# Optimization experiments

Hardware: AMD Instinct MI355X
Metric: run time of the kernel (lower is better)

## Reference

```python
import math
import jax, jax.numpy as jnp
import numpy as np

D_MODEL = 1024
D_STATE = 16
D_CONV = 4
EXPAND = 2
N_MOD = 2
D_INNER = EXPAND * D_MODEL
DT_RANK = math.ceil(D_MODEL / 16)
B_SZ = 2
SEQLEN = 2048


def setup_inputs() -> dict:
    key = jax.random.key(0)
    ks = jax.random.split(key, 10)
    hidden_states = jax.random.normal(ks[0], (B_SZ, SEQLEN, D_MODEL), jnp.float32)
    modality_ids = jax.random.randint(ks[1], (B_SZ, SEQLEN), 0, N_MOD).astype(jnp.int32)
    W_in = jax.random.normal(ks[2], (N_MOD, 2 * D_INNER, D_MODEL), jnp.float32) * (D_MODEL ** -0.5)
    conv_w = jax.random.normal(ks[3], (D_INNER, D_CONV), jnp.float32) * (D_CONV ** -0.5)
    conv_b = jnp.zeros((D_INNER,), jnp.float32)
    W_x = jax.random.normal(ks[4], (N_MOD, DT_RANK + 2 * D_STATE, D_INNER), jnp.float32) * (D_INNER ** -0.5)
    dt_init_std = DT_RANK ** -0.5
    W_dt = jax.random.uniform(ks[5], (N_MOD, D_INNER, DT_RANK), jnp.float32, -dt_init_std, dt_init_std)
    # dt bias init: inverse-softplus of dt ~ LogUniform(dt_min, dt_max), per Mamba
    dt = jnp.exp(jax.random.uniform(ks[6], (N_MOD, D_INNER), jnp.float32)
                 * (math.log(0.1) - math.log(0.001)) + math.log(0.001))
    dt = jnp.maximum(dt, 1e-4)
    b_dt = dt + jnp.log(-jnp.expm1(-dt))
    A_log = jnp.log(jnp.broadcast_to(jnp.arange(1, D_STATE + 1, dtype=jnp.float32), (D_INNER, D_STATE)))
    D = jnp.ones((D_INNER,), jnp.float32)
    W_out = jax.random.normal(ks[7], (N_MOD, D_MODEL, D_INNER), jnp.float32) * (D_INNER ** -0.5)
    return dict(hidden_states=hidden_states, modality_ids=modality_ids, W_in=W_in,
                conv_w=conv_w, conv_b=conv_b, W_x=W_x, W_dt=W_dt, b_dt=b_dt,
                A_log=A_log, D=D, W_out=W_out)


def _expert_apply(x, W, ids):
    # x: [T, d_in], W: [E, d_out, d_in], ids: [T] -> per-token expert output [T, d_out]
    all_out = jnp.einsum('td,eod->teo', x, W)
    return jnp.take_along_axis(all_out, ids[:, None, None], axis=1)[:, 0, :]


def _forward(hidden_states, modality_ids, W_in, conv_w, conv_b, W_x, W_dt, b_dt, A_log, D, W_out):
    Bsz, L, d_model = hidden_states.shape
    d_inner, d_state = A_log.shape
    dt_rank = W_dt.shape[2]
    d_conv = conv_w.shape[1]
    ids = modality_ids.reshape(-1)  # [T]

    # per-modality in_proj dispatch/combine
    xz = _expert_apply(hidden_states.reshape(-1, d_model), W_in, ids)  # [T, 2*d_inner]
    xz = xz.reshape(Bsz, L, 2 * d_inner).transpose(0, 2, 1)            # [B, 2*d_inner, L]
    x, z = jnp.split(xz, 2, axis=1)                                    # [B, d_inner, L] each

    # causal depthwise conv1d (pad left d_conv-1, truncate to L) + SiLU
    xp = jnp.pad(x, ((0, 0), (0, 0), (d_conv - 1, 0)))
    xc = conv_b[None, :, None]
    for k in range(d_conv):
        xc = xc + conv_w[None, :, k:k + 1] * xp[:, :, k:k + L]
    x = jax.nn.silu(xc)

    # per-modality x_proj -> (dt, B, C)
    xt = x.transpose(0, 2, 1).reshape(-1, d_inner)                     # [T, d_inner]
    x_dbl = _expert_apply(xt, W_x, ids)
    dt, Bm, Cm = jnp.split(x_dbl, [dt_rank, dt_rank + d_state], axis=-1)

    # per-modality dt_proj (with bias), then softplus (delta_softplus=True)
    dt = _expert_apply(dt, W_dt, ids) + b_dt[ids]                      # [T, d_inner]
    dt = jax.nn.softplus(dt)

    A = -jnp.exp(A_log)                                                # [d_inner, d_state]

    # selective scan over sequence (time-major)
    dts = dt.reshape(Bsz, L, d_inner).transpose(1, 0, 2)               # [L, B, d_inner]
    Bms = Bm.reshape(Bsz, L, d_state).transpose(1, 0, 2)               # [L, B, d_state]
    Cms = Cm.reshape(Bsz, L, d_state).transpose(1, 0, 2)               # [L, B, d_state]
    xs = x.transpose(2, 0, 1)                                          # [L, B, d_inner]

    def step(state, inp):
        x_t, dt_t, B_t, C_t = inp
        dA = jnp.exp(dt_t[..., None] * A)                              # [B, d_inner, d_state]
        state = state * dA + (dt_t * x_t)[..., None] * B_t[:, None, :]
        y_t = jnp.einsum('bdn,bn->bd', state, C_t)
        return state, y_t

    init = jnp.zeros((Bsz, d_inner, d_state), jnp.float32)
    _, ys = jax.lax.scan(step, init, (xs, dts, Bms, Cms))              # ys: [L, B, d_inner]

    y = ys.transpose(1, 0, 2)                                          # [B, L, d_inner]
    y = y + x.transpose(0, 2, 1) * D[None, None, :]                    # skip D*u
    y = y * jax.nn.silu(z.transpose(0, 2, 1))                          # z gate

    # per-modality out_proj
    out = _expert_apply(y.reshape(-1, d_inner), W_out, ids)
    return out.reshape(Bsz, L, d_model)


def reference(hidden_states, modality_ids, W_in, conv_w, conv_b, W_x, W_dt, b_dt, A_log, D, W_out):
    return _forward(hidden_states, modality_ids, W_in, conv_w, conv_b, W_x, W_dt, b_dt, A_log, D, W_out)
```

## Files before the change

### kernel.cpp

```cpp
#include <hip/hip_runtime.h>
#include <hip/hip_bf16.h>
#include <math.h>

#define B_SZ 2
#define SEQLEN 2048
#define D_MODEL 1024
#define D_INNER 2048
#define D_STATE 16
#define D_CONV 4
#define DT_RANK 64
#define NTOK (B_SZ * SEQLEN)
#define XDBL 96
#define NC 32
#define LC 64
#define PADTOT (17 * 256)

typedef float f32x4 __attribute__((ext_vector_type(4)));
typedef unsigned int u32x4 __attribute__((ext_vector_type(4)));
typedef __hip_bfloat16 bf16;

__device__ __forceinline__ float siluf(float v) { return v / (1.f + __expf(-v)); }
__device__ __forceinline__ float softplusf(float v) { return (v > 20.f) ? v : log1pf(__expf(v)); }

__device__ __forceinline__ void mfma_bf16(f32x4& acc, u32x4 a, u32x4 b) {
  asm volatile("v_mfma_f32_16x16x32_bf16 %0, %1, %2, %0" : "+v"(acc) : "v"(a), "v"(b));
}

__device__ __forceinline__ void gload16(const bf16* g, bf16* l) {
  __builtin_amdgcn_global_load_lds(
      (const __attribute__((address_space(1))) unsigned int*)g,
      (__attribute__((address_space(3))) unsigned int*)l, 16, 0, 0);
}

__global__ __launch_bounds__(1024) void k_perm(const int* __restrict__ ids, int* __restrict__ perm) {
  __shared__ int sc[1024];
  const int tid = threadIdx.x;
  int loc[4];
  int cnt = 0;
#pragma unroll
  for (int q = 0; q < 4; q++) {
    loc[q] = ids[tid * 4 + q];
    cnt += (loc[q] == 0);
  }
  sc[tid] = cnt;
  __syncthreads();
  for (int off = 1; off < 1024; off <<= 1) {
    int v = sc[tid];
    int u = (tid >= off) ? sc[tid - off] : 0;
    __syncthreads();
    sc[tid] = v + u;
    __syncthreads();
  }
  const int N0 = sc[1023];
  const int m0 = (N0 + 255) & ~255;
  const int N1 = NTOK - N0;
  for (int idx = tid; idx < PADTOT; idx += 1024)
    if ((idx >= N0 && idx < m0) || idx >= m0 + N1) perm[idx] = -1;
  int zb = sc[tid] - cnt;
#pragma unroll
  for (int q = 0; q < 4; q++) {
    int t = tid * 4 + q;
    if (loc[q] == 0) { perm[zb] = t; zb++; }
    else             { perm[m0 + (t - zb)] = t; }
  }
}

#define CVT_H   (NTOK * D_MODEL)
#define CVT_WIN (2 * 2 * D_INNER * D_MODEL)
#define CVT_WX  (2 * XDBL * D_INNER)
#define CVT_WDT (2 * D_INNER * DT_RANK)
#define CVT_WO  (2 * D_MODEL * D_INNER)
#define CVT_TOT (CVT_H + CVT_WIN + CVT_WX + CVT_WDT + CVT_WO)
__global__ __launch_bounds__(256) void k_cvtall(const float* __restrict__ h,
                                                const float* __restrict__ Win,
                                                const float* __restrict__ Wx,
                                                const float* __restrict__ Wdt,
                                                const float* __restrict__ Wout,
                                                bf16* __restrict__ hB, bf16* __restrict__ WinB,
                                                bf16* __restrict__ WxB, bf16* __restrict__ WdtB,
                                                bf16* __restrict__ WoB) {
  size_t i = ((size_t)blockIdx.x * 256 + threadIdx.x) * 8;
  const float* src; bf16* dst; size_t off;
  if (i < CVT_H)                          { src = h;    dst = hB;   off = i; }
  else if (i < CVT_H + CVT_WIN)           { src = Win;  dst = WinB; off = i - CVT_H; }
  else if (i < CVT_H + CVT_WIN + CVT_WX)  { src = Wx;   dst = WxB;  off = i - CVT_H - CVT_WIN; }
  else if (i < CVT_TOT - CVT_WO)          { src = Wdt;  dst = WdtB; off = i - CVT_H - CVT_WIN - CVT_WX; }
  else                                    { src = Wout; dst = WoB;  off = i - (CVT_TOT - CVT_WO); }
  float4 f0 = *(const float4*)&src[off];
  float4 f1 = *(const float4*)&src[off + 4];
  __align__(16) bf16 tmp[8];
  tmp[0] = __float2bfloat16(f0.x); tmp[1] = __float2bfloat16(f0.y);
  tmp[2] = __float2bfloat16(f0.z); tmp[3] = __float2bfloat16(f0.w);
  tmp[4] = __float2bfloat16(f1.x); tmp[5] = __float2bfloat16(f1.y);
  tmp[6] = __float2bfloat16(f1.z); tmp[7] = __float2bfloat16(f1.w);
  *(u32x4*)&dst[off] = *(const u32x4*)tmp;
}

template <int KDIM, int NW, int KSPLIT, int EPI>
__device__ __forceinline__ void gemmP_body(const bf16* __restrict__ actB,
                                           const int* __restrict__ perm,
                                           const int* __restrict__ ids,
                                           const bf16* __restrict__ WB,
                                           bf16* __restrict__ outx,
                                           bf16* __restrict__ outz,
                                           float* __restrict__ out0) {
  constexpr int KLEN = KDIM / KSPLIT;
  constexpr int NT = KLEN / 64;
  constexpr int NCOL = (EPI == 1) ? (D_MODEL / 128) : 0;
  __shared__ bf16 As[3][256 * 64];
  __shared__ bf16 Ws[3][128 * 64];
  const int tid = threadIdx.x;

  const int gx = gridDim.x;
  const int nwg = gx * gridDim.y;
  const int fid = blockIdx.y * gx + blockIdx.x;
  const int q8 = nwg >> 3;
  const int swz = (fid & 7) * q8 + (fid >> 3);
  const int bx = swz % gx, by = swz / gx;
  const int ot = (KSPLIT > 1) ? (bx % NCOL) * 128 : bx * 128;
  const int kz = (KSPLIT > 1) ? bx / NCOL : 0;
  const int kbase = kz * KLEN;
  const int tt = by * 256;

  const int lane = tid & 63, w = tid >> 6;
  const int wr = w >> 1, wc = w & 1;
  const int lr = lane & 15, lg = lane >> 4;

  const int t00 = perm[tt];
  const int eu = (t00 >= 0) ? ids[t00] : 0;
  const size_t wexp = (size_t)eu * NW * KDIM;

  const int kswz = ((lane & 7) ^ ((lane >> 3) & 7)) * 8;
  size_t aBase[4]; int aLds[4];
  size_t bBase[2]; int bLds[2];
#pragma unroll
  for (int v = 0; v < 4; v++) {
    const int row = w * 32 + v * 8 + (lane >> 3);
    int ta = perm[tt + row]; if (ta < 0) ta = 0;
    aBase[v] = (size_t)ta * KDIM + kswz;
    aLds[v] = (w * 32 + v * 8) * 64;
  }
#pragma unroll
  for (int v = 0; v < 2; v++) {
    const int row = w * 16 + v * 8 + (lane >> 3);
    bBase[v] = wexp + (size_t)(ot + row) * KDIM + kswz;
    bLds[v] = (w * 16 + v * 8) * 64;
  }

  f32x4 acc[4][4];
#pragma unroll
  for (int i = 0; i < 4; i++)
#pragma unroll
    for (int j = 0; j < 4; j++) acc[i][j] = (f32x4){0.f, 0.f, 0.f, 0.f};

#pragma unroll
  for (int kt = 0; kt < 2; kt++) {
    const int k0 = kbase + kt * 64;
    gload16(&actB[aBase[0] + k0], &As[kt][aLds[0]]);
    gload16(&actB[aBase[1] + k0], &As[kt][aLds[1]]);
    gload16(&actB[aBase[2] + k0], &As[kt][aLds[2]]);
    gload16(&actB[aBase[3] + k0], &As[kt][aLds[3]]);
    gload16(&WB[bBase[0] + k0], &Ws[kt][bLds[0]]);
    gload16(&WB[bBase[1] + k0], &Ws[kt][bLds[1]]);
  }

  int bR = 0, bS = 2;
  for (int kt = 0; kt < NT; ++kt) {
    const int kp = kbase + (kt + 2) * 64;
    const bool st = (kt + 2 < NT);
    if (st) {
      gload16(&actB[aBase[0] + kp], &As[bS][aLds[0]]);
      gload16(&actB[aBase[1] + kp], &As[bS][aLds[1]]);
      gload16(&WB[bBase[0] + kp], &Ws[bS][bLds[0]]);
    }
    if (kt < NT - 2)       asm volatile("s_waitcnt vmcnt(9)" ::: "memory");
    else if (kt == NT - 2) asm volatile("s_waitcnt vmcnt(6)" ::: "memory");
    else                   asm volatile("s_waitcnt vmcnt(0)" ::: "memory");
    asm volatile("s_barrier" ::: "memory");

    const bf16* Ab = As[bR];
    const bf16* Wb = Ws[bR];
    u32x4 a[4][2], b0[2][2];
#pragma unroll
    for (int f = 0; f < 4; f++)
#pragma unroll
      for (int s = 0; s < 2; s++) {
        const int row = wr * 64 + f * 16 + lr;
        a[f][s] = *(const u32x4*)&Ab[row * 64 + ((s * 4 + lg) ^ (row & 7)) * 8];
      }
#pragma unroll
    for (int j = 0; j < 2; j++)
#pragma unroll
      for (int s = 0; s < 2; s++) {
        const int row = wc * 64 + j * 16 + lr;
        b0[j][s] = *(const u32x4*)&Wb[row * 64 + ((s * 4 + lg) ^ (row & 7)) * 8];
      }
    __builtin_amdgcn_s_setprio(1);
#pragma unroll
    for (int f = 0; f < 4; f++)
#pragma unroll
      for (int j = 0; j < 2; j++) {
        mfma_bf16(acc[f][j], a[f][0], b0[j][0]);
        mfma_bf16(acc[f][j], a[f][1], b0[j][1]);
      }
    __builtin_amdgcn_s_setprio(0);

    if (st) {
      gload16(&actB[aBase[2] + kp], &As[bS][aLds[2]]);
      gload16(&actB[aBase[3] + kp], &As[bS][aLds[3]]);
      gload16(&WB[bBase[1] + kp], &Ws[bS][bLds[1]]);
    }
    u32x4 b1[2][2];
#pragma unroll
    for (int j = 0; j < 2; j++)
#pragma unroll
      for (int s = 0; s < 2; s++) {
        const int row = wc * 64 + (2 + j) * 16 + lr;
        b1[j][s] = *(const u32x4*)&Wb[row * 64 + ((s * 4 + lg) ^ (row & 7)) * 8];
      }
    __builtin_amdgcn_s_setprio(1);
#pragma unroll
    for (int f = 0; f < 4; f++)
#pragma unroll
      for (int j = 0; j < 2; j++) {
        mfma_bf16(acc[f][2 + j], a[f][0], b1[j][0]);
        mfma_bf16(acc[f][2 + j], a[f][1], b1[j][1]);
      }
    __builtin_amdgcn_s_setprio(0);
    asm volatile("s_waitcnt lgkmcnt(0)" ::: "memory");
    asm volatile("s_barrier" ::: "memory");
    bR = (bR == 2) ? 0 : bR + 1;
    bS = (bS == 2) ? 0 : bS + 1;
  }

#pragma unroll
  for (int i = 0; i < 4; i++) {
#pragma unroll
    for (int r = 0; r < 4; r++) {
      const int m = wr * 64 + i * 16 + lg * 4 + r;
      const int t = perm[tt + m];
      if (t < 0) continue;
#pragma unroll
      for (int j = 0; j < 4; j++) {
        const int col = ot + wc * 64 + j * 16 + lr;
        const float v = acc[i][j][r];
        if (EPI == 0) {
          const bf16 vb = __float2bfloat16(v);
          if (col < D_INNER) outx[(size_t)t * D_INNER + col] = vb;
          else outz[(size_t)t * D_INNER + (col - D_INNER)] = vb;
        } else {
          out0[((size_t)kz * NTOK + t) * D_MODEL + col] = v;
        }
      }
    }
  }
}

__global__ __launch_bounds__(512) void k_inproj(const bf16* actB, const int* perm, const int* ids,
                                                const bf16* WB, bf16* outx, bf16* outz) {
  gemmP_body<D_MODEL, 2 * D_INNER, 1, 0>(actB, perm, ids, WB, outx, outz, nullptr);
}
__global__ __launch_bounds__(512) void k_outproj(const bf16* actB, const int* perm, const int* ids,
                                                 const bf16* WB, float* out0) {
  gemmP_body<D_INNER, D_MODEL, 2, 1>(actB, perm, ids, WB, nullptr, nullptr, out0);
}

__global__ __launch_bounds__(256) void k_xdblg(const bf16* __restrict__ actB,
                                               const int* __restrict__ perm,
                                               const int* __restrict__ ids,
                                               const bf16* __restrict__ WB,
                                               float* __restrict__ out0) {
  constexpr int KDIM = D_INNER, NW = XDBL, LDO = XDBL, KSPLIT = 8;
  constexpr int KLEN = KDIM / KSPLIT;
  __shared__ bf16 As[128 * 64];
  __shared__ bf16 Ws[128 * 64];
  __shared__ int permL[128];
  const int tid = threadIdx.x;
  const int bx = blockIdx.x, by = blockIdx.y;

  const int ot = 0;
  const int kz = bx;
  const int kbase = kz * KLEN;
  const int tt = by * 128;

  if (tid < 128) permL[tid] = perm[tt + tid];

  const int lane = tid & 63, w = tid >> 6;
  const int wr = w >> 1, wc = w & 1;
  const int lr = lane & 15, lg = lane >> 4;

  const int t00 = perm[tt];
  const int eu = (t00 >= 0) ? ids[t00] : 0;
  const size_t wexp = (size_t)eu * NW * KDIM;

  const int srow = w * 32 + (lane >> 3);
  const int scol = (lane & 7) * 8;
  size_t abase[4], bbase[4];
  int ldsoff[4];
#pragma unroll
  for (int v = 0; v < 4; v++) {
    const int row = srow + v * 8;
    int ta = perm[tt + row];
    if (ta < 0) ta = 0;
    abase[v] = (size_t)ta * KDIM + scol;
    int orow = ot + row;
    orow = (orow < NW) ? orow : (NW - 1);
    bbase[v] = wexp + (size_t)orow * KDIM + scol;
    ldsoff[v] = (w * 32 + v * 8) * 64;
  }

  f32x4 acc[4][4];
#pragma unroll
  for (int i = 0; i < 4; i++)
#pragma unroll
    for (int j = 0; j < 4; j++) acc[i][j] = (f32x4){0.f, 0.f, 0.f, 0.f};

  for (int k0 = kbase; k0 < kbase + KLEN; k0 += 64) {
#pragma unroll
    for (int v = 0; v < 4; v++) {
      gload16(&actB[abase[v] + k0], &As[ldsoff[v]]);
      gload16(&WB[bbase[v] + k0], &Ws[ldsoff[v]]);
    }
    __syncthreads();
#pragma unroll
    for (int ks = 0; ks < 64; ks += 32) {
      u32x4 a[4], b[4];
#pragma unroll
      for (int f = 0; f < 4; f++)
        a[f] = *(const u32x4*)&As[(wr * 64 + f * 16 + lr) * 64 + ks + lg * 8];
#pragma unroll
      for (int f = 0; f < 4; f++)
        b[f] = *(const u32x4*)&Ws[(wc * 64 + f * 16 + lr) * 64 + ks + lg * 8];
#pragma unroll
      for (int i = 0; i < 4; i++)
#pragma unroll
        for (int j = 0; j < 4; j++) mfma_bf16(acc[i][j], a[i], b[j]);
    }
    __syncthreads();
  }

#pragma unroll
  for (int i = 0; i < 4; i++) {
#pragma unroll
    for (int r = 0; r < 4; r++) {
      const int m = wr * 64 + i * 16 + lg * 4 + r;
      const int t = permL[m];
      if (t < 0) continue;
#pragma unroll
      for (int j = 0; j < 4; j++) {
        const int col = ot + wc * 64 + j * 16 + lr;
        if (col < NW) out0[((size_t)kz * NTOK + t) * LDO + col] = acc[i][j][r];
      }
    }
  }
}

__global__ __launch_bounds__(256) void k_dtv(const float* __restrict__ xdbl,
                                             const int* __restrict__ perm,
                                             const int* __restrict__ ids,
                                             const float* __restrict__ Wdt,
                                             const float* __restrict__ bdt,
                                             bf16* __restrict__ dtB) {
  const int tid = threadIdx.x;
  const int idx = blockIdx.y * 256 + tid;
  int t = perm[idx];
  const bool act = (t >= 0);
  if (!act) t = 0;
  const int t0 = perm[blockIdx.y * 256];
  const int e = (t0 >= 0) ? ids[t0] : 0;
  float xs[64];
#pragma unroll
  for (int k4 = 0; k4 < 16; k4++) {
    float4 v = *(const float4*)&xdbl[(size_t)t * XDBL + k4 * 4];
    xs[k4 * 4 + 0] = v.x; xs[k4 * 4 + 1] = v.y;
    xs[k4 * 4 + 2] = v.z; xs[k4 * 4 + 3] = v.w;
  }
  const int cbase = blockIdx.x * 64;
  const float* Wb = Wdt + ((size_t)e * D_INNER + cbase) * DT_RANK;
  const float* bb = bdt + (size_t)e * D_INNER + cbase;
#pragma unroll 1
  for (int cc = 0; cc < 8; cc++) {
    __align__(16) bf16 outv[8];
#pragma unroll
    for (int c8 = 0; c8 < 8; c8++) {
      const int c = cc * 8 + c8;
      const float* wrow = Wb + (size_t)c * DT_RANK;
      float acc = bb[c];
#pragma unroll
      for (int k = 0; k < 64; k++) acc = fmaf(xs[k], wrow[k], acc);
      outv[c8] = __float2bfloat16(softplusf(acc));
    }
    if (act) *(u32x4*)&dtB[(size_t)t * D_INNER + cbase + cc * 8] = *(const u32x4*)outv;
  }
}

__global__ __launch_bounds__(256) void k_xred(const float* __restrict__ part,
                                              float* __restrict__ xdbl) {
  const int i = blockIdx.x * 256 + threadIdx.x;
  float s = 0.f;
#pragma unroll
  for (int k = 0; k < 8; k++) s += part[(size_t)k * NTOK * XDBL + i];
  xdbl[i] = s;
}

__global__ __launch_bounds__(256) void k_ored2(const float* __restrict__ part,
                                               float* __restrict__ out) {
  const size_t base = ((size_t)blockIdx.x * 256 + threadIdx.x) * 4;
  constexpr size_t NM = (size_t)NTOK * D_MODEL;
  float4 s = *(const float4*)&part[base];
  float4 p = *(const float4*)&part[NM + base];
  s.x += p.x; s.y += p.y; s.z += p.z; s.w += p.w;
  *(float4*)&out[base] = s;
}

__global__ __launch_bounds__(256) void k_conv(const bf16* __restrict__ xrawB,
                                              const float* __restrict__ cw,
                                              const float* __restrict__ cb,
                                              bf16* __restrict__ xB) {
  int idx = blockIdx.x * 256 + threadIdx.x;
  int c = idx & (D_INNER - 1);
  int t = idx >> 11;
  int l = t & (SEQLEN - 1);
  int b = t >> 11;
  float acc = cb[c];
#pragma unroll
  for (int k = 0; k < D_CONV; k++) {
    int ll = l + k - (D_CONV - 1);
    if (ll >= 0)
      acc = fmaf(cw[c * D_CONV + k],
                 __bfloat162float(xrawB[((size_t)(b * SEQLEN + ll)) * D_INNER + c]), acc);
  }
  xB[(size_t)idx] = __float2bfloat16(siluf(acc));
}

__global__ __launch_bounds__(256) void k_scan_part(const bf16* __restrict__ xB,
                                                   const bf16* __restrict__ dtB,
                                                   const float* __restrict__ xdbl,
                                                   const float* __restrict__ A_log,
                                                   float* __restrict__ F,
                                                   float* __restrict__ Sdt) {
  __shared__ float Bs[LC][D_STATE];
  const int tid = threadIdx.x;
  const int j = blockIdx.y;
  const int ch = blockIdx.x * 256 + tid;
  const int b = ch >> 11, c = ch & (D_INNER - 1);
  const int t0 = (b << 11) + j * LC;
  {
    int l = tid >> 2, q = (tid & 3) * 4;
    *(float4*)&Bs[l][q] = *(const float4*)&xdbl[(size_t)(t0 + l) * XDBL + DT_RANK + q];
  }
  float Ar[D_STATE];
#pragma unroll
  for (int n4 = 0; n4 < 4; n4++) {
    float4 a = *(const float4*)&A_log[(size_t)c * D_STATE + n4 * 4];
    Ar[n4 * 4 + 0] = -__expf(a.x); Ar[n4 * 4 + 1] = -__expf(a.y);
    Ar[n4 * 4 + 2] = -__expf(a.z); Ar[n4 * 4 + 3] = -__expf(a.w);
  }
  __syncthreads();
  float st[D_STATE];
#pragma unroll
  for (int n = 0; n < D_STATE; n++) st[n] = 0.f;
  float sdt = 0.f;
  float dtc = __bfloat162float(dtB[(size_t)t0 * D_INNER + c]);
  float xc = __bfloat162float(xB[(size_t)t0 * D_INNER + c]);
  for (int l = 0; l < LC; l++) {
    float dtn = 0.f, xn = 0.f;
    if (l < LC - 1) {
      dtn = __bfloat162float(dtB[(size_t)(t0 + l + 1) * D_INNER + c]);
      xn = __bfloat162float(xB[(size_t)(t0 + l + 1) * D_INNER + c]);
    }
    const float dtx = dtc * xc;
    sdt += dtc;
#pragma unroll
    for (int n = 0; n < D_STATE; n++) {
      float dA = __expf(dtc * Ar[n]);
      st[n] = fmaf(st[n], dA, dtx * Bs[l][n]);
    }
    dtc = dtn; xc = xn;
  }
  const size_t fb = ((size_t)j * NTOK + ch) * D_STATE;
#pragma unroll
  for (int n4 = 0; n4 < 4; n4++)
    *(float4*)&F[fb + n4 * 4] = make_float4(st[n4 * 4], st[n4 * 4 + 1], st[n4 * 4 + 2], st[n4 * 4 + 3]);
  Sdt[(size_t)j * NTOK + ch] = sdt;
}

__global__ __launch_bounds__(256) void k_combine(const float* __restrict__ F,
                                                 const float* __restrict__ Sdt,
                                                 const float* __restrict__ A_log,
                                                 float* __restrict__ s0) {
  const int gid = blockIdx.x * 256 + threadIdx.x;
  const int ch = gid >> 4, n = gid & 15, c = ch & (D_INNER - 1);
  const float Ar = -__expf(A_log[(size_t)c * D_STATE + n]);
  float s = 0.f;
  for (int j = 0; j < NC; j++) {
    s0[((size_t)j * NTOK + ch) * D_STATE + n] = s;
    s = fmaf(s, __expf(Ar * Sdt[(size_t)j * NTOK + ch]), F[((size_t)j * NTOK + ch) * D_STATE + n]);
  }
}

__global__ __launch_bounds__(256) void k_scan_fin(const bf16* __restrict__ xB,
                                                  const bf16* __restrict__ dtB,
                                                  const float* __restrict__ xdbl,
                                                  const bf16* __restrict__ zB,
                                                  const float* __restrict__ A_log,
                                                  const float* __restrict__ Dp,
                                                  const float* __restrict__ s0,
                                                  bf16* __restrict__ ybuf) {
  __shared__ float Bs[LC][D_STATE];
  __shared__ float Cs[LC][D_STATE];
  const int tid = threadIdx.x;
  const int j = blockIdx.y;
  const int ch = blockIdx.x * 256 + tid;
  const int b = ch >> 11, c = ch & (D_INNER - 1);
  const int t0 = (b << 11) + j * LC;
  {
    int l = tid >> 2, q = (tid & 3) * 4;
    *(float4*)&Bs[l][q] = *(const float4*)&xdbl[(size_t)(t0 + l) * XDBL + DT_RANK + q];
    *(float4*)&Cs[l][q] = *(const float4*)&xdbl[(size_t)(t0 + l) * XDBL + DT_RANK + D_STATE + q];
  }
  float Ar[D_STATE];
#pragma unroll
  for (int n4 = 0; n4 < 4; n4++) {
    float4 a = *(const float4*)&A_log[(size_t)c * D_STATE + n4 * 4];
    Ar[n4 * 4 + 0] = -__expf(a.x); Ar[n4 * 4 + 1] = -__expf(a.y);
    Ar[n4 * 4 + 2] = -__expf(a.z); Ar[n4 * 4 + 3] = -__expf(a.w);
  }
  __syncthreads();
  float st[D_STATE];
  const size_t sb = ((size_t)j * NTOK + ch) * D_STATE;
#pragma unroll
  for (int n4 = 0; n4 < 4; n4++) {
    float4 s = *(const float4*)&s0[sb + n4 * 4];
    st[n4 * 4 + 0] = s.x; st[n4 * 4 + 1] = s.y; st[n4 * 4 + 2] = s.z; st[n4 * 4 + 3] = s.w;
  }
  const float Dc = Dp[c];
  float dtc = __bfloat162float(dtB[(size_t)t0 * D_INNER + c]);
  float xc = __bfloat162float(xB[(size_t)t0 * D_INNER + c]);
  for (int l = 0; l < LC; l++) {
    float dtn = 0.f, xn = 0.f;
    if (l < LC - 1) {
      dtn = __bfloat162float(dtB[(size_t)(t0 + l + 1) * D_INNER + c]);
      xn = __bfloat162float(xB[(size_t)(t0 + l + 1) * D_INNER + c]);
    }
    const float zv = __bfloat162float(zB[(size_t)(t0 + l) * D_INNER + c]);
    const float dtx = dtc * xc;
    float y = 0.f;
#pragma unroll
    for (int n = 0; n < D_STATE; n++) {
      float dA = __expf(dtc * Ar[n]);
      st[n] = fmaf(st[n], dA, dtx * Bs[l][n]);
      y = fmaf(st[n], Cs[l][n], y);
    }
    float yv = fmaf(xc, Dc, y);
    ybuf[(size_t)(t0 + l) * D_INNER + c] = __float2bfloat16(yv * siluf(zv));
    dtc = dtn; xc = xn;
  }
}

extern "C" void kernel_launch(void* const* d_in, const int* in_sizes, int n_in,
                              void* d_out, int out_size, void* d_ws, size_t ws_size,
                              hipStream_t stream) {
  const float* h = (const float*)d_in[0];
  const int* ids = (const int*)d_in[1];
  const float* Win = (const float*)d_in[2];
  const float* cw = (const float*)d_in[3];
  const float* cb = (const float*)d_in[4];
  const float* Wx = (const float*)d_in[5];
  const float* Wdt = (const float*)d_in[6];
  const float* bdt = (const float*)d_in[7];
  const float* Alog = (const float*)d_in[8];
  const float* Dp = (const float*)d_in[9];
  const float* Wout = (const float*)d_in[10];
  float* out = (float*)d_out;

  const size_t NTD = (size_t)NTOK * D_INNER;
  float* ws = (float*)d_ws;
  float* slot0 = ws + 0 * NTD;
  float* slot1 = ws + 1 * NTD;
  float* slot2 = ws + 2 * NTD;
  float* slot3 = ws + 3 * NTD;
  size_t cur = 4 * NTD;
  float* xdbl_p = ws + cur; cur += (size_t)NTOK * XDBL;
  float* sdt_p = ws + cur; cur += (size_t)NC * NTOK;
  int* perm = (int*)(ws + cur); cur += PADTOT;
  bf16* xB = (bf16*)(ws + cur); cur += NTD / 2;
  bf16* WoB = (bf16*)(ws + cur); cur += CVT_WO / 2;
  bf16* WxB = (bf16*)(ws + cur); cur += CVT_WX / 2;
  bf16* WdtB = (bf16*)(ws + cur); cur += CVT_WDT / 2;

  bf16* hB = (bf16*)slot0;
  bf16* dtbB = (bf16*)slot0;
  bf16* zB = (bf16*)slot1;
  bf16* WinB = (bf16*)slot2;
  float* part = slot2;
  float* part2 = slot1;
  bf16* xrawB = (bf16*)slot3;
  float* F = slot3;
  bf16* yB = (bf16*)slot3;
  float* s0 = (float*)d_out;

  k_perm<<<1, 1024, 0, stream>>>(ids, perm);
  k_cvtall<<<CVT_TOT / 8 / 256, 256, 0, stream>>>(h, Win, Wx, Wdt, Wout, hB, WinB, WxB, WdtB, WoB);
  k_inproj<<<dim3(32, 17), 512, 0, stream>>>(hB, perm, ids, WinB, xrawB, zB);
  k_conv<<<NTD / 256, 256, 0, stream>>>(xrawB, cw, cb, xB);
  k_xdblg<<<dim3(8, 34), 256, 0, stream>>>(xB, perm, ids, WxB, part);
  k_xred<<<NTOK * XDBL / 256, 256, 0, stream>>>(part, xdbl_p);
  k_dtv<<<dim3(32, 17), 256, 0, stream>>>(xdbl_p, perm, ids, Wdt, bdt, dtbB);
  k_scan_part<<<dim3(16, NC), 256, 0, stream>>>(xB, dtbB, xdbl_p, Alog, F, sdt_p);
  k_combine<<<256, 256, 0, stream>>>(F, sdt_p, Alog, s0);
  k_scan_fin<<<dim3(16, NC), 256, 0, stream>>>(xB, dtbB, xdbl_p, zB, Alog, Dp, s0, yB);
  k_outproj<<<dim3(16, 17), 512, 0, stream>>>(yB, perm, ids, WoB, part2);
  k_ored2<<<NTOK * D_MODEL / 4 / 256, 256, 0, stream>>>(part2, out);
}
```

Before: 365.9 us.

## Tile dt projection through shared memory with 4x4 register blocking

```diff
diff --git a/kernel.cpp b/kernel.cpp
--- a/kernel.cpp
+++ b/kernel.cpp
@@ -361,36 +361,59 @@
                                              const float* __restrict__ Wdt,
                                              const float* __restrict__ bdt,
                                              bf16* __restrict__ dtB) {
+  __shared__ float Xs[64][65];
+  __shared__ float Ws[64][65];
+  __shared__ int permL[64];
   const int tid = threadIdx.x;
-  const int idx = blockIdx.y * 256 + tid;
-  int t = perm[idx];
-  const bool act = (t >= 0);
-  if (!act) t = 0;
-  const int t0 = perm[blockIdx.y * 256];
+  const int tt = blockIdx.y * 64;
+  const int cb = blockIdx.x * 64;
+  if (tid < 64) permL[tid] = perm[tt + tid];
+  const int t0 = perm[tt];
   const int e = (t0 >= 0) ? ids[t0] : 0;
-  float xs[64];
+  {
+    const int r = tid >> 2, q = (tid & 3) * 16;
+    int ta = perm[tt + r];
+    if (ta < 0) ta = 0;
+    const float* xsrc = &xdbl[(size_t)ta * XDBL + q];
+    const float* wsrc = &Wdt[((size_t)e * D_INNER + cb + r) * DT_RANK + q];
+#pragma unroll
+    for (int u = 0; u < 4; u++) {
+      float4 xv = *(const float4*)&xsrc[u * 4];
+      float4 wv = *(const float4*)&wsrc[u * 4];
+      *(float4*)&Xs[r][q + u * 4] = xv;
+      *(float4*)&Ws[r][q + u * 4] = wv;
+    }
+  }
+  __syncthreads();
+  const int tl = (tid & 15) * 4;
+  const int cl = (tid >> 4) * 4;
+  float acc[4][4] = {};
 #pragma unroll
   for (int k4 = 0; k4 < 16; k4++) {
-    float4 v = *(const float4*)&xdbl[(size_t)t * XDBL + k4 * 4];
-    xs[k4 * 4 + 0] = v.x; xs[k4 * 4 + 1] = v.y;
-    xs[k4 * 4 + 2] = v.z; xs[k4 * 4 + 3] = v.w;
-  }
-  const int cbase = blockIdx.x * 64;
-  const float* Wb = Wdt + ((size_t)e * D_INNER + cbase) * DT_RANK;
-  const float* bb = bdt + (size_t)e * D_INNER + cbase;
-#pragma unroll 1
-  for (int cc = 0; cc < 8; cc++) {
-    __align__(16) bf16 outv[8];
-#pragma unroll
-    for (int c8 = 0; c8 < 8; c8++) {
-      const int c = cc * 8 + c8;
-      const float* wrow = Wb + (size_t)c * DT_RANK;
-      float acc = bb[c];
-#pragma unroll
-      for (int k = 0; k < 64; k++) acc = fmaf(xs[k], wrow[k], acc);
-      outv[c8] = __float2bfloat16(softplusf(acc));
-    }
-    if (act) *(u32x4*)&dtB[(size_t)t * D_INNER + cbase + cc * 8] = *(const u32x4*)outv;
+    float4 xv[4], wv[4];
+#pragma unroll
+    for (int i = 0; i < 4; i++) xv[i] = *(const float4*)&Xs[tl + i][k4 * 4];
+#pragma unroll
+    for (int j = 0; j < 4; j++) wv[j] = *(const float4*)&Ws[cl + j][k4 * 4];
+#pragma unroll
+    for (int i = 0; i < 4; i++)
+#pragma unroll
+      for (int j = 0; j < 4; j++) {
+        acc[i][j] = fmaf(xv[i].x, wv[j].x, acc[i][j]);
+        acc[i][j] = fmaf(xv[i].y, wv[j].y, acc[i][j]);
+        acc[i][j] = fmaf(xv[i].z, wv[j].z, acc[i][j]);
+        acc[i][j] = fmaf(xv[i].w, wv[j].w, acc[i][j]);
+      }
+  }
+#pragma unroll
+  for (int i = 0; i < 4; i++) {
+    const int t = permL[tl + i];
+    if (t < 0) continue;
+    __align__(8) bf16 ov[4];
+#pragma unroll
+    for (int j = 0; j < 4; j++)
+      ov[j] = __float2bfloat16(softplusf(acc[i][j] + bdt[e * D_INNER + cb + cl + j]));
+    *(uint2*)&dtB[(size_t)t * D_INNER + cb + cl] = *(const uint2*)ov;
   }
 }
 
@@ -606,7 +629,7 @@
   k_conv<<<NTD / 256, 256, 0, stream>>>(xrawB, cw, cb, xB);
   k_xdblg<<<dim3(8, 34), 256, 0, stream>>>(xB, perm, ids, WxB, part);
   k_xred<<<NTOK * XDBL / 256, 256, 0, stream>>>(part, xdbl_p);
-  k_dtv<<<dim3(32, 17), 256, 0, stream>>>(xdbl_p, perm, ids, Wdt, bdt, dtbB);
+  k_dtv<<<dim3(32, PADTOT / 64), 256, 0, stream>>>(xdbl_p, perm, ids, Wdt, bdt, dtbB);
   k_scan_part<<<dim3(16, NC), 256, 0, stream>>>(xB, dtbB, xdbl_p, Alog, F, sdt_p);
   k_combine<<<256, 256, 0, stream>>>(F, sdt_p, Alog, s0);
   k_scan_fin<<<dim3(16, NC), 256, 0, stream>>>(xB, dtbB, xdbl_p, zB, Alog, Dp, s0, yB);
```

Result: slower. 408.7 us (+11.7%).
